# Performance work log

Measured on AMD Instinct MI355X. Metric: run time of the kernel, lower is better.

Reference implementation:

```python
import jax, jax.numpy as jnp
import numpy as np

N_NODES = 100000
N_EDGES = 1200000
N_GRAPHS = 512


def _init_linear(key, fan_in, fan_out):
    kw, kb = jax.random.split(key)
    lim = 1.0 / np.sqrt(fan_in)
    W = jax.random.uniform(kw, (fan_in, fan_out), minval=-lim, maxval=lim, dtype=jnp.float32)
    b = jax.random.uniform(kb, (fan_out,), minval=-lim, maxval=lim, dtype=jnp.float32)
    return W, b


def setup_inputs() -> dict:
    key = jax.random.key(0)
    ks = jax.random.split(key, 12)
    x = jax.random.normal(ks[0], (N_NODES, 10), dtype=jnp.float32)
    edge_index = jax.random.randint(ks[1], (2, N_EDGES), 0, N_NODES, dtype=jnp.int64)
    batch = jnp.sort(jax.random.randint(ks[2], (N_NODES,), 0, N_GRAPHS, dtype=jnp.int64))
    edge_weights = jax.random.uniform(ks[3], (N_EDGES,), dtype=jnp.float32)
    W1, b1 = _init_linear(ks[4], 10, 60)
    W2, b2 = _init_linear(ks[5], 60, 60)
    W3, b3 = _init_linear(ks[6], 60, 60)
    W4, b4 = _init_linear(ks[7], 60, 60)
    L1w, L1b = _init_linear(ks[8], 60, 60)
    L2w, L2b = _init_linear(ks[9], 60, 10)
    L3w, L3b = _init_linear(ks[10], 10, 2)
    return dict(x=x, edge_index=edge_index, batch=batch, edge_weights=edge_weights,
                W1=W1, b1=b1, W2=W2, b2=b2, W3=W3, b3=b3, W4=W4, b4=b4,
                L1w=L1w, L1b=L1b, L2w=L2w, L2b=L2b, L3w=L3w, L3b=L3b)


def gcn_conv(x, W, b, src, dst, ew, n):
    # PyG GCNConv: add self-loops (weight 1), symmetric normalization, linear, scatter-add.
    deg = jax.ops.segment_sum(ew, dst, num_segments=n) + 1.0  # +1 self-loop
    dinv = jnp.where(deg > 0, jax.lax.rsqrt(deg), 0.0)
    h = x @ W  # [n, out]
    norm = dinv[src] * ew * dinv[dst]  # [E]
    agg = jax.ops.segment_sum(h[src] * norm[:, None], dst, num_segments=n)
    agg = agg + h * (dinv * dinv)[:, None]  # self-loop contribution (weight 1)
    return agg + b


def _forward(x, edge_index, batch, edge_weights,
             W1, b1, W2, b2, W3, b3, W4, b4,
             L1w, L1b, L2w, L2b, L3w, L3b):
    src, dst = edge_index[0], edge_index[1]
    n = x.shape[0]
    h = jax.nn.relu(gcn_conv(x, W1, b1, src, dst, edge_weights, n))
    h = jax.nn.relu(gcn_conv(h, W2, b2, src, dst, edge_weights, n))
    h = jax.nn.relu(gcn_conv(h, W3, b3, src, dst, edge_weights, n))
    h = jax.nn.relu(gcn_conv(h, W4, b4, src, dst, edge_weights, n))
    g = jax.ops.segment_max(h, batch, num_segments=N_GRAPHS)
    g = jnp.where(jnp.isfinite(g), g, 0.0)  # guard empty graphs
    g = jax.nn.relu(g @ L1w + L1b)
    g = jax.nn.relu(g @ L2w + L2b)
    return g @ L3w + L3b


def reference(x, edge_index, batch, edge_weights,
              W1, b1, W2, b2, W3, b3, W4, b4,
              L1w, L1b, L2w, L2b, L3w, L3b):
    return _forward(x, edge_index, batch, edge_weights,
                    W1, b1, W2, b2, W3, b3, W4, b4,
                    L1w, L1b, L2w, L2b, L3w, L3b)
```

## Files before the change

kernel.cpp:

```cpp
#include <hip/hip_runtime.h>
#include <hip/hip_fp16.h>

#define N_NODES 100000
#define N_EDGES 1200000
#define N_GRAPHS 512
#define F 60
#define NPW 8
#define CAP 48
#define NBKT 782
#define EPB 4096
#define CPX 37
#define NCH 296
#define BKT_CAP 2048

__global__ void __launch_bounds__(256) k_hist(const int* __restrict__ dst,
                                              int* __restrict__ histM, int E) {
    __shared__ int h[NBKT];
    int c = (blockIdx.x & 7) * CPX + (blockIdx.x >> 3);
    for (int i = threadIdx.x; i < NBKT; i += 256) h[i] = 0;
    __syncthreads();
    int b0 = c * EPB;
    for (int i = threadIdx.x; i < EPB; i += 256) {
        int e = b0 + i;
        if (e < E) atomicAdd(&h[dst[e] >> 7], 1);
    }
    __syncthreads();
    for (int i = threadIdx.x; i < NBKT; i += 256) histM[c * NBKT + i] = h[i];
}

__global__ void k_scan(int* __restrict__ histM, int* __restrict__ tot) {
    int b = blockIdx.x * 256 + threadIdx.x;
    if (b >= NBKT) return;
    int running = 0;
    for (int c = 0; c < NCH; c += 8) {
        int i0 = (c + 0) * NBKT + b, i1 = (c + 1) * NBKT + b;
        int i2 = (c + 2) * NBKT + b, i3 = (c + 3) * NBKT + b;
        int i4 = (c + 4) * NBKT + b, i5 = (c + 5) * NBKT + b;
        int i6 = (c + 6) * NBKT + b, i7 = (c + 7) * NBKT + b;
        int v0 = histM[i0], v1 = histM[i1], v2 = histM[i2], v3 = histM[i3];
        int v4 = histM[i4], v5 = histM[i5], v6 = histM[i6], v7 = histM[i7];
        histM[i0] = running; running += v0;
        histM[i1] = running; running += v1;
        histM[i2] = running; running += v2;
        histM[i3] = running; running += v3;
        histM[i4] = running; running += v4;
        histM[i5] = running; running += v5;
        histM[i6] = running; running += v6;
        histM[i7] = running; running += v7;
    }
    tot[b] = running;
}

__global__ void __launch_bounds__(256) k_fill(const int* __restrict__ src,
                                              const int* __restrict__ dst,
                                              const float* __restrict__ ew,
                                              const int* __restrict__ histM,
                                              int2* __restrict__ bkt, int E) {
    __shared__ int h[NBKT];
    int c = (blockIdx.x & 7) * CPX + (blockIdx.x >> 3);
    for (int i = threadIdx.x; i < NBKT; i += 256) h[i] = 0;
    __syncthreads();
    int b0 = c * EPB;
    const int* bas = histM + c * NBKT;
    for (int i = threadIdx.x; i < EPB; i += 256) {
        int e = b0 + i;
        if (e >= E) continue;
        int d = dst[e];
        int b = d >> 7;
        int r = atomicAdd(&h[b], 1);
        int pos = bas[b] + r;
        if (pos < BKT_CAP) {
            int2 p;
            p.x = src[e] | ((d & 127) << 17);
            p.y = __float_as_int(ew[e]);
            bkt[(size_t)b * BKT_CAP + pos] = p;
        }
    }
}

__global__ void __launch_bounds__(256) k_build(
        const int* __restrict__ tot, const int2* __restrict__ bkt,
        int2* __restrict__ csr, int* __restrict__ cnt,
        float* __restrict__ dinv, const float* __restrict__ x,
        float* __restrict__ xs, int n) {
    __shared__ int lcur[128];
    __shared__ float ldeg[128];
    int b = blockIdx.x, tid = threadIdx.x;
    if (tid < 128) { lcur[tid] = 0; ldeg[tid] = 0.f; }
    __syncthreads();
    int nbase = b << 7;
    int m = min(tot[b], BKT_CAP);
    const int2* sb = bkt + (size_t)b * BKT_CAP;
    for (int i = tid; i < m; i += 256) {
        int2 p = sb[i];
        int srcv = p.x & 0x1FFFF;
        int low = (p.x >> 17) & 127;
        int pos = atomicAdd(&lcur[low], 1);
        if (pos < CAP) {
            int2 q; q.x = srcv; q.y = p.y;
            csr[(size_t)(nbase + low) * CAP + pos] = q;
        }
        atomicAdd(&ldeg[low], __int_as_float(p.y));
    }
    __syncthreads();
    if (tid < 128) {
        int v = nbase + tid;
        if (v < n) {
            int mA = min(lcur[tid], CAP);
            cnt[v] = mA;
            float di = rsqrtf(ldeg[tid] + 1.0f);
            dinv[v] = di;
            #pragma unroll
            for (int c2 = 0; c2 < 10; ++c2) xs[v * 16 + c2] = di * x[v * 10 + c2];
            #pragma unroll
            for (int c2 = 10; c2 < 16; ++c2) xs[v * 16 + c2] = 0.f;
            int g0 = tid & ~3;
            int m4 = max(max(min(lcur[g0], CAP),     min(lcur[g0 + 1], CAP)),
                         max(min(lcur[g0 + 2], CAP), min(lcur[g0 + 3], CAP)));
            int R = (m4 + 7) & ~7;
            int2 z; z.x = 0; z.y = 0;
            for (int e = mA; e < R; ++e) csr[(size_t)v * CAP + e] = z;
        }
    }
}

template<bool FIRST, bool SCALE_OUT>
__global__ void __launch_bounds__(256) k_layer(
        const void* __restrict__ HinV, const float* __restrict__ W,
        const float* __restrict__ bias,
        const int2* __restrict__ csr, const int* __restrict__ cnt,
        const float* __restrict__ dinv,
        __half* __restrict__ Hout, int n) {
    constexpr int WIN = FIRST ? 10 : 60;
    constexpr int WINP = FIRST ? 12 : 60;
    const float*  Hf = (const float*)HinV;
    const __half* Hh = (const __half*)HinV;
    __shared__ float Ws[WINP * 64];
    __shared__ __align__(16) float accS[4][NPW][64];
    for (int i = threadIdx.x; i < WINP * 64; i += 256) {
        int k = i >> 6, j = i & 63;
        Ws[i] = (j < F && k < WIN) ? W[k * F + j] : 0.f;
    }

    int wave = threadIdx.x >> 6;
    int lane = threadIdx.x & 63;
    float bj = (lane < F) ? bias[lane] : 0.f;
    int base = (blockIdx.x * 4 + wave) * NPW;

    if constexpr (FIRST) {
        __syncthreads();
        int l16 = lane & 15;
        int q = lane >> 4;
        #pragma unroll
        for (int p = 0; p < 2; ++p) {
            int v = base + 4 * p + q;
            float a = Hf[v * 16 + l16];
            int mm = min(cnt[v], CAP);
            int t1 = max(mm, __shfl_xor(mm, 16));
            int mu = max(t1, __shfl_xor(t1, 32));
            const int2* seg = csr + (size_t)v * CAP;
            for (int e = 0; e < mu; e += 4) {
                int2 p0 = seg[e], p1 = seg[e + 1], p2 = seg[e + 2], p3 = seg[e + 3];
                float x0 = Hf[p0.x * 16 + l16];
                float x1 = Hf[p1.x * 16 + l16];
                float x2 = Hf[p2.x * 16 + l16];
                float x3 = Hf[p3.x * 16 + l16];
                a = fmaf(__int_as_float(p0.y), x0, a);
                a = fmaf(__int_as_float(p1.y), x1, a);
                a = fmaf(__int_as_float(p2.y), x2, a);
                a = fmaf(__int_as_float(p3.y), x3, a);
            }
            accS[wave][4 * p + q][l16] = a * dinv[v];
        }
        float o[NPW];
        #pragma unroll
        for (int t = 0; t < NPW; ++t) o[t] = bj;
        const float4* aq = (const float4*)&accS[wave][0][0];
        #pragma unroll
        for (int kq = 0; kq < 3; ++kq) {
            float w0 = Ws[(4 * kq + 0) * 64 + lane];
            float w1 = Ws[(4 * kq + 1) * 64 + lane];
            float w2 = Ws[(4 * kq + 2) * 64 + lane];
            float w3 = Ws[(4 * kq + 3) * 64 + lane];
            #pragma unroll
            for (int t = 0; t < NPW; ++t) {
                float4 aa = aq[t * 16 + kq];
                o[t] = fmaf(aa.x, w0, o[t]);
                o[t] = fmaf(aa.y, w1, o[t]);
                o[t] = fmaf(aa.z, w2, o[t]);
                o[t] = fmaf(aa.w, w3, o[t]);
            }
        }
        #pragma unroll
        for (int t = 0; t < NPW; ++t) {
            float sc = SCALE_OUT ? dinv[base + t] : 1.f;
            Hout[(size_t)(base + t) * 64 + lane] = __float2half_rn(fmaxf(o[t], 0.f) * sc);
        }
    } else {
        __syncthreads();
        int h  = lane >> 5;
        int lh = lane & 31;
        int fo = lh * 2;

        #pragma unroll
        for (int p = 0; p < 4; ++p) {
            int v = base + 2 * p + h;
            float di = dinv[v];
            __half2 sh = *(const __half2*)(Hh + (size_t)v * 64 + fo);
            float2 a;
            a.x = __low2float(sh);
            a.y = __high2float(sh);
            int mm = min(cnt[v], CAP);
            int mo = __shfl(mm, lane ^ 32);
            int mu = max(mm, mo);
            const int2* seg = csr + (size_t)v * CAP;
            for (int e = 0; e < mu; e += 8) {
                const int4* s4 = (const int4*)(seg + e);
                int4 q0 = s4[0], q1 = s4[1], q2 = s4[2], q3 = s4[3];
                __half2 g0 = *(const __half2*)(Hh + (size_t)q0.x * 64 + fo);
                __half2 g1 = *(const __half2*)(Hh + (size_t)q0.z * 64 + fo);
                __half2 g2 = *(const __half2*)(Hh + (size_t)q1.x * 64 + fo);
                __half2 g3 = *(const __half2*)(Hh + (size_t)q1.z * 64 + fo);
                __half2 g4 = *(const __half2*)(Hh + (size_t)q2.x * 64 + fo);
                __half2 g5 = *(const __half2*)(Hh + (size_t)q2.z * 64 + fo);
                __half2 g6 = *(const __half2*)(Hh + (size_t)q3.x * 64 + fo);
                __half2 g7 = *(const __half2*)(Hh + (size_t)q3.z * 64 + fo);
                float w0 = __int_as_float(q0.y), w1 = __int_as_float(q0.w);
                float w2 = __int_as_float(q1.y), w3 = __int_as_float(q1.w);
                float w4 = __int_as_float(q2.y), w5 = __int_as_float(q2.w);
                float w6 = __int_as_float(q3.y), w7 = __int_as_float(q3.w);
                a.x = fmaf(w0, __low2float(g0), a.x); a.y = fmaf(w0, __high2float(g0), a.y);
                a.x = fmaf(w1, __low2float(g1), a.x); a.y = fmaf(w1, __high2float(g1), a.y);
                a.x = fmaf(w2, __low2float(g2), a.x); a.y = fmaf(w2, __high2float(g2), a.y);
                a.x = fmaf(w3, __low2float(g3), a.x); a.y = fmaf(w3, __high2float(g3), a.y);
                a.x = fmaf(w4, __low2float(g4), a.x); a.y = fmaf(w4, __high2float(g4), a.y);
                a.x = fmaf(w5, __low2float(g5), a.x); a.y = fmaf(w5, __high2float(g5), a.y);
                a.x = fmaf(w6, __low2float(g6), a.x); a.y = fmaf(w6, __high2float(g6), a.y);
                a.x = fmaf(w7, __low2float(g7), a.x); a.y = fmaf(w7, __high2float(g7), a.y);
            }
            a.x *= di; a.y *= di;
            *(float2*)&accS[wave][2 * p + h][fo] = a;
        }

        float o[NPW];
        #pragma unroll
        for (int t = 0; t < NPW; ++t) o[t] = bj;
        const float4* aq = (const float4*)&accS[wave][0][0];
        #pragma unroll
        for (int kq = 0; kq < 15; ++kq) {
            float w0 = Ws[(4 * kq + 0) * 64 + lane];
            float w1 = Ws[(4 * kq + 1) * 64 + lane];
            float w2 = Ws[(4 * kq + 2) * 64 + lane];
            float w3 = Ws[(4 * kq + 3) * 64 + lane];
            #pragma unroll
            for (int t = 0; t < NPW; ++t) {
                float4 aa = aq[t * 16 + kq];
                o[t] = fmaf(aa.x, w0, o[t]);
                o[t] = fmaf(aa.y, w1, o[t]);
                o[t] = fmaf(aa.z, w2, o[t]);
                o[t] = fmaf(aa.w, w3, o[t]);
            }
        }
        #pragma unroll
        for (int t = 0; t < NPW; ++t) {
            float sc = SCALE_OUT ? dinv[base + t] : 1.f;
            Hout[(size_t)(base + t) * 64 + lane] = __float2half_rn(fmaxf(o[t], 0.f) * sc);
        }
    }
}

__global__ void k_gstart(const int* __restrict__ batch, int* __restrict__ start, int n) {
    int i = blockIdx.x * 256 + threadIdx.x;
    if (i >= n) return;
    int b = batch[i];
    int pb = (i == 0) ? -1 : batch[i - 1];
    for (int g = pb + 1; g <= b; ++g) start[g] = i;
    if (i == n - 1) for (int g = b + 1; g <= N_GRAPHS; ++g) start[g] = n;
}

__global__ void k_pool2(const __half* __restrict__ H, const int* __restrict__ start,
                        float* __restrict__ g) {
    __shared__ float red[4 * F];
    int gi = blockIdx.x;
    int wave = threadIdx.x >> 6;
    int lane = threadIdx.x & 63;
    int s = start[gi], e = start[gi + 1];
    float m = 0.f;
    for (int i = s + wave; i < e; i += 4)
        m = fmaxf(m, __half2float(H[(size_t)i * 64 + lane]));
    if (lane < F) red[wave * F + lane] = m;
    __syncthreads();
    if (threadIdx.x < F) {
        float r = fmaxf(fmaxf(red[threadIdx.x], red[F + threadIdx.x]),
                        fmaxf(red[2 * F + threadIdx.x], red[3 * F + threadIdx.x]));
        g[gi * F + threadIdx.x] = r;
    }
}

__global__ void k_mlp(const float* __restrict__ g,
                      const float* __restrict__ L1w, const float* __restrict__ L1b,
                      const float* __restrict__ L2w, const float* __restrict__ L2b,
                      const float* __restrict__ L3w, const float* __restrict__ L3b,
                      float* __restrict__ out) {
    __shared__ float gin[F], h1[F], h2[10];
    int gi = blockIdx.x;
    int t = threadIdx.x;
    if (t < F) gin[t] = g[gi * F + t];
    __syncthreads();
    if (t < F) {
        float a = L1b[t];
        for (int k = 0; k < F; ++k) a += gin[k] * L1w[k * F + t];
        h1[t] = fmaxf(a, 0.f);
    }
    __syncthreads();
    if (t < 10) {
        float a = L2b[t];
        for (int k = 0; k < F; ++k) a += h1[k] * L2w[k * 10 + t];
        h2[t] = fmaxf(a, 0.f);
    }
    __syncthreads();
    if (t < 2) {
        float a = L3b[t];
        for (int k = 0; k < 10; ++k) a += h2[k] * L3w[k * 2 + t];
        out[gi * 2 + t] = a;
    }
}

extern "C" void kernel_launch(void* const* d_in, const int* in_sizes, int n_in,
                              void* d_out, int out_size, void* d_ws, size_t ws_size,
                              hipStream_t stream) {
    const int n = N_NODES, E = N_EDGES;
    const float* x   = (const float*)d_in[0];
    const int* ei    = (const int*)d_in[1];
    const int* batch = (const int*)d_in[2];
    const float* ew  = (const float*)d_in[3];
    const float* W1 = (const float*)d_in[4],  *b1 = (const float*)d_in[5];
    const float* W2 = (const float*)d_in[6],  *b2 = (const float*)d_in[7];
    const float* W3 = (const float*)d_in[8],  *b3 = (const float*)d_in[9];
    const float* W4 = (const float*)d_in[10], *b4 = (const float*)d_in[11];
    const float* L1w = (const float*)d_in[12], *L1b = (const float*)d_in[13];
    const float* L2w = (const float*)d_in[14], *L2b = (const float*)d_in[15];
    const float* L3w = (const float*)d_in[16], *L3b = (const float*)d_in[17];
    float* out = (float*)d_out;

    const int* src = ei;
    const int* dst = ei + E;

    char* ws = (char*)d_ws;
    size_t off = 0;
    auto carve = [&](size_t bytes) {
        void* p = ws + off;
        off += (bytes + 255) & ~size_t(255);
        return p;
    };
    int*    cnt   = (int*)carve(n * 4);
    float*  dinv  = (float*)carve(n * 4);
    int*    gst   = (int*)carve((N_GRAPHS + 1) * 4);
    int2*   csr   = (int2*)carve((size_t)n * CAP * 8);
    int2*   bkt   = (int2*)carve((size_t)NBKT * BKT_CAP * 8);
    int*    histM = (int*)carve((size_t)NCH * NBKT * 4);
    int*    tot   = (int*)carve(NBKT * 4);
    float*  xs    = (float*)carve((size_t)n * 16 * 4);
    __half* hA    = (__half*)carve((size_t)n * 64 * 2);
    __half* hB    = (__half*)carve((size_t)n * 64 * 2);
    float*  g0    = (float*)carve((size_t)N_GRAPHS * F * 4);
    (void)ws_size;

    const int NB = (n + 255) / 256;
    const int LB = n / (4 * NPW);

    k_hist<<<NCH, 256, 0, stream>>>(dst, histM, E);
    k_scan<<<(NBKT + 255) / 256, 256, 0, stream>>>(histM, tot);
    k_fill<<<NCH, 256, 0, stream>>>(src, dst, ew, histM, bkt, E);
    k_build<<<NBKT, 256, 0, stream>>>(tot, bkt, csr, cnt, dinv, x, xs, n);
    k_gstart<<<NB, 256, 0, stream>>>(batch, gst, n);

    k_layer<true,  true ><<<LB, 256, 0, stream>>>(xs, W1, b1, csr, cnt, dinv, hA, n);
    k_layer<false, true ><<<LB, 256, 0, stream>>>(hA, W2, b2, csr, cnt, dinv, hB, n);
    k_layer<false, true ><<<LB, 256, 0, stream>>>(hB, W3, b3, csr, cnt, dinv, hA, n);
    k_layer<false, false><<<LB, 256, 0, stream>>>(hA, W4, b4, csr, cnt, dinv, hB, n);

    k_pool2<<<N_GRAPHS, 256, 0, stream>>>(hB, gst, g0);
    k_mlp<<<N_GRAPHS, 64, 0, stream>>>(g0, L1w, L1b, L2w, L2b, L3w, L3b, out);
}
```

Measured before the change: 253.9 us.

## Pack CSR entries into 32-bit words with quantized weights and fuse small kernels

CSR edges now fit in one 32-bit word: 17-bit source index and 15-bit fixed-point edge weight. This halves the CSR bytes read in every layer. The hidden layers now gather for four nodes at once under a shared loop bound, padded to groups of 8 nodes, which raises memory-level parallelism. The scan is fused with graph-start computation and pooling is fused with the MLP, removing two launches. Quantizing weights to 15 bits adds rounding error, and the shared loop bound adds wasted iterations for low-degree nodes.

```diff
diff --git a/kernel.cpp b/kernel.cpp
--- a/kernel.cpp
+++ b/kernel.cpp
@@ -12,6 +12,7 @@
 #define CPX 37
 #define NCH 296
 #define BKT_CAP 2048
+#define WSC 3.0518509e-05f
 
 __global__ void __launch_bounds__(256) k_hist(const int* __restrict__ dst,
                                               int* __restrict__ histM, int E) {
@@ -28,27 +29,38 @@
     for (int i = threadIdx.x; i < NBKT; i += 256) histM[c * NBKT + i] = h[i];
 }
 
-__global__ void k_scan(int* __restrict__ histM, int* __restrict__ tot) {
-    int b = blockIdx.x * 256 + threadIdx.x;
-    if (b >= NBKT) return;
-    int running = 0;
-    for (int c = 0; c < NCH; c += 8) {
-        int i0 = (c + 0) * NBKT + b, i1 = (c + 1) * NBKT + b;
-        int i2 = (c + 2) * NBKT + b, i3 = (c + 3) * NBKT + b;
-        int i4 = (c + 4) * NBKT + b, i5 = (c + 5) * NBKT + b;
-        int i6 = (c + 6) * NBKT + b, i7 = (c + 7) * NBKT + b;
-        int v0 = histM[i0], v1 = histM[i1], v2 = histM[i2], v3 = histM[i3];
-        int v4 = histM[i4], v5 = histM[i5], v6 = histM[i6], v7 = histM[i7];
-        histM[i0] = running; running += v0;
-        histM[i1] = running; running += v1;
-        histM[i2] = running; running += v2;
-        histM[i3] = running; running += v3;
-        histM[i4] = running; running += v4;
-        histM[i5] = running; running += v5;
-        histM[i6] = running; running += v6;
-        histM[i7] = running; running += v7;
-    }
-    tot[b] = running;
+__global__ void k_scan_gstart(int* __restrict__ histM, int* __restrict__ tot,
+                              const int* __restrict__ batch, int* __restrict__ gst, int n) {
+    int bi = blockIdx.x;
+    if (bi < 4) {
+        int b = bi * 256 + threadIdx.x;
+        if (b >= NBKT) return;
+        int running = 0;
+        for (int c = 0; c < NCH; c += 8) {
+            int i0 = (c + 0) * NBKT + b, i1 = (c + 1) * NBKT + b;
+            int i2 = (c + 2) * NBKT + b, i3 = (c + 3) * NBKT + b;
+            int i4 = (c + 4) * NBKT + b, i5 = (c + 5) * NBKT + b;
+            int i6 = (c + 6) * NBKT + b, i7 = (c + 7) * NBKT + b;
+            int v0 = histM[i0], v1 = histM[i1], v2 = histM[i2], v3 = histM[i3];
+            int v4 = histM[i4], v5 = histM[i5], v6 = histM[i6], v7 = histM[i7];
+            histM[i0] = running; running += v0;
+            histM[i1] = running; running += v1;
+            histM[i2] = running; running += v2;
+            histM[i3] = running; running += v3;
+            histM[i4] = running; running += v4;
+            histM[i5] = running; running += v5;
+            histM[i6] = running; running += v6;
+            histM[i7] = running; running += v7;
+        }
+        tot[b] = running;
+    } else {
+        int i = (bi - 4) * 256 + threadIdx.x;
+        if (i >= n) return;
+        int b = batch[i];
+        int pb = (i == 0) ? -1 : batch[i - 1];
+        for (int g = pb + 1; g <= b; ++g) gst[g] = i;
+        if (i == n - 1) for (int g = b + 1; g <= N_GRAPHS; ++g) gst[g] = n;
+    }
 }
 
 __global__ void __launch_bounds__(256) k_fill(const int* __restrict__ src,
@@ -80,7 +92,7 @@
 
 __global__ void __launch_bounds__(256) k_build(
         const int* __restrict__ tot, const int2* __restrict__ bkt,
-        int2* __restrict__ csr, int* __restrict__ cnt,
+        unsigned* __restrict__ csr, int* __restrict__ cnt,
         float* __restrict__ dinv, const float* __restrict__ x,
         float* __restrict__ xs, int n) {
     __shared__ int lcur[128];
@@ -97,8 +109,8 @@
         int low = (p.x >> 17) & 127;
         int pos = atomicAdd(&lcur[low], 1);
         if (pos < CAP) {
-            int2 q; q.x = srcv; q.y = p.y;
-            csr[(size_t)(nbase + low) * CAP + pos] = q;
+            unsigned w15 = (unsigned)(int)rintf(__int_as_float(p.y) * 32767.f);
+            csr[(size_t)(nbase + low) * CAP + pos] = (unsigned)srcv | (w15 << 17);
         }
         atomicAdd(&ldeg[low], __int_as_float(p.y));
     }
@@ -114,12 +126,12 @@
             for (int c2 = 0; c2 < 10; ++c2) xs[v * 16 + c2] = di * x[v * 10 + c2];
             #pragma unroll
             for (int c2 = 10; c2 < 16; ++c2) xs[v * 16 + c2] = 0.f;
-            int g0 = tid & ~3;
-            int m4 = max(max(min(lcur[g0], CAP),     min(lcur[g0 + 1], CAP)),
-                         max(min(lcur[g0 + 2], CAP), min(lcur[g0 + 3], CAP)));
-            int R = (m4 + 7) & ~7;
-            int2 z; z.x = 0; z.y = 0;
-            for (int e = mA; e < R; ++e) csr[(size_t)v * CAP + e] = z;
+            int g0 = tid & ~7;
+            int m8 = 0;
+            #pragma unroll
+            for (int i2 = 0; i2 < 8; ++i2) m8 = max(m8, min(lcur[g0 + i2], CAP));
+            int R = (m8 + 3) & ~3;
+            for (int e = mA; e < R; ++e) csr[(size_t)v * CAP + e] = 0u;
         }
     }
 }
@@ -128,7 +140,7 @@
 __global__ void __launch_bounds__(256) k_layer(
         const void* __restrict__ HinV, const float* __restrict__ W,
         const float* __restrict__ bias,
-        const int2* __restrict__ csr, const int* __restrict__ cnt,
+        const unsigned* __restrict__ csr, const int* __restrict__ cnt,
         const float* __restrict__ dinv,
         __half* __restrict__ Hout, int n) {
     constexpr int WIN = FIRST ? 10 : 60;
@@ -155,20 +167,20 @@
         for (int p = 0; p < 2; ++p) {
             int v = base + 4 * p + q;
             float a = Hf[v * 16 + l16];
-            int mm = min(cnt[v], CAP);
+            int mm = cnt[v];
             int t1 = max(mm, __shfl_xor(mm, 16));
             int mu = max(t1, __shfl_xor(t1, 32));
-            const int2* seg = csr + (size_t)v * CAP;
+            const unsigned* seg = csr + (size_t)v * CAP;
             for (int e = 0; e < mu; e += 4) {
-                int2 p0 = seg[e], p1 = seg[e + 1], p2 = seg[e + 2], p3 = seg[e + 3];
-                float x0 = Hf[p0.x * 16 + l16];
-                float x1 = Hf[p1.x * 16 + l16];
-                float x2 = Hf[p2.x * 16 + l16];
-                float x3 = Hf[p3.x * 16 + l16];
-                a = fmaf(__int_as_float(p0.y), x0, a);
-                a = fmaf(__int_as_float(p1.y), x1, a);
-                a = fmaf(__int_as_float(p2.y), x2, a);
-                a = fmaf(__int_as_float(p3.y), x3, a);
+                uint4 qq = *(const uint4*)(seg + e);
+                float x0 = Hf[(qq.x & 0x1FFFF) * 16 + l16];
+                float x1 = Hf[(qq.y & 0x1FFFF) * 16 + l16];
+                float x2 = Hf[(qq.z & 0x1FFFF) * 16 + l16];
+                float x3 = Hf[(qq.w & 0x1FFFF) * 16 + l16];
+                a = fmaf((float)(qq.x >> 17) * WSC, x0, a);
+                a = fmaf((float)(qq.y >> 17) * WSC, x1, a);
+                a = fmaf((float)(qq.z >> 17) * WSC, x2, a);
+                a = fmaf((float)(qq.w >> 17) * WSC, x3, a);
             }
             accS[wave][4 * p + q][l16] = a * dinv[v];
         }
@@ -202,44 +214,52 @@
         int lh = lane & 31;
         int fo = lh * 2;
 
+        float2 acc2[4];
+        float dis[4];
+        const unsigned* seg[4];
         #pragma unroll
         for (int p = 0; p < 4; ++p) {
             int v = base + 2 * p + h;
-            float di = dinv[v];
+            dis[p] = dinv[v];
             __half2 sh = *(const __half2*)(Hh + (size_t)v * 64 + fo);
-            float2 a;
-            a.x = __low2float(sh);
-            a.y = __high2float(sh);
-            int mm = min(cnt[v], CAP);
-            int mo = __shfl(mm, lane ^ 32);
-            int mu = max(mm, mo);
-            const int2* seg = csr + (size_t)v * CAP;
-            for (int e = 0; e < mu; e += 8) {
-                const int4* s4 = (const int4*)(seg + e);
-                int4 q0 = s4[0], q1 = s4[1], q2 = s4[2], q3 = s4[3];
-                __half2 g0 = *(const __half2*)(Hh + (size_t)q0.x * 64 + fo);
-                __half2 g1 = *(const __half2*)(Hh + (size_t)q0.z * 64 + fo);
-                __half2 g2 = *(const __half2*)(Hh + (size_t)q1.x * 64 + fo);
-                __half2 g3 = *(const __half2*)(Hh + (size_t)q1.z * 64 + fo);
-                __half2 g4 = *(const __half2*)(Hh + (size_t)q2.x * 64 + fo);
-                __half2 g5 = *(const __half2*)(Hh + (size_t)q2.z * 64 + fo);
-                __half2 g6 = *(const __half2*)(Hh + (size_t)q3.x * 64 + fo);
-                __half2 g7 = *(const __half2*)(Hh + (size_t)q3.z * 64 + fo);
-                float w0 = __int_as_float(q0.y), w1 = __int_as_float(q0.w);
-                float w2 = __int_as_float(q1.y), w3 = __int_as_float(q1.w);
-                float w4 = __int_as_float(q2.y), w5 = __int_as_float(q2.w);
-                float w6 = __int_as_float(q3.y), w7 = __int_as_float(q3.w);
-                a.x = fmaf(w0, __low2float(g0), a.x); a.y = fmaf(w0, __high2float(g0), a.y);
-                a.x = fmaf(w1, __low2float(g1), a.x); a.y = fmaf(w1, __high2float(g1), a.y);
-                a.x = fmaf(w2, __low2float(g2), a.x); a.y = fmaf(w2, __high2float(g2), a.y);
-                a.x = fmaf(w3, __low2float(g3), a.x); a.y = fmaf(w3, __high2float(g3), a.y);
-                a.x = fmaf(w4, __low2float(g4), a.x); a.y = fmaf(w4, __high2float(g4), a.y);
-                a.x = fmaf(w5, __low2float(g5), a.x); a.y = fmaf(w5, __high2float(g5), a.y);
-                a.x = fmaf(w6, __low2float(g6), a.x); a.y = fmaf(w6, __high2float(g6), a.y);
-                a.x = fmaf(w7, __low2float(g7), a.x); a.y = fmaf(w7, __high2float(g7), a.y);
+            acc2[p].x = __low2float(sh);
+            acc2[p].y = __high2float(sh);
+            seg[p] = csr + (size_t)v * CAP;
+        }
+        int cmy = cnt[base + (lane & 7)];
+        int m1 = max(cmy, __shfl_xor(cmy, 1));
+        int m2 = max(m1, __shfl_xor(m1, 2));
+        int mu = max(m2, __shfl_xor(m2, 4));
+
+        for (int e = 0; e < mu; e += 4) {
+            uint4 q[4];
+            #pragma unroll
+            for (int p = 0; p < 4; ++p) q[p] = *(const uint4*)(seg[p] + e);
+            #pragma unroll
+            for (int p = 0; p < 4; ++p) {
+                unsigned e0 = q[p].x, e1 = q[p].y, e2 = q[p].z, e3 = q[p].w;
+                __half2 g0 = *(const __half2*)(Hh + (size_t)(e0 & 0x1FFFF) * 64 + fo);
+                __half2 g1 = *(const __half2*)(Hh + (size_t)(e1 & 0x1FFFF) * 64 + fo);
+                __half2 g2 = *(const __half2*)(Hh + (size_t)(e2 & 0x1FFFF) * 64 + fo);
+                __half2 g3 = *(const __half2*)(Hh + (size_t)(e3 & 0x1FFFF) * 64 + fo);
+                float w0 = (float)(e0 >> 17) * WSC;
+                float w1 = (float)(e1 >> 17) * WSC;
+                float w2 = (float)(e2 >> 17) * WSC;
+                float w3 = (float)(e3 >> 17) * WSC;
+                acc2[p].x = fmaf(w0, __low2float(g0), acc2[p].x);
+                acc2[p].y = fmaf(w0, __high2float(g0), acc2[p].y);
+                acc2[p].x = fmaf(w1, __low2float(g1), acc2[p].x);
+                acc2[p].y = fmaf(w1, __high2float(g1), acc2[p].y);
+                acc2[p].x = fmaf(w2, __low2float(g2), acc2[p].x);
+                acc2[p].y = fmaf(w2, __high2float(g2), acc2[p].y);
+                acc2[p].x = fmaf(w3, __low2float(g3), acc2[p].x);
+                acc2[p].y = fmaf(w3, __high2float(g3), acc2[p].y);
             }
-            a.x *= di; a.y *= di;
-            *(float2*)&accS[wave][2 * p + h][fo] = a;
+        }
+        #pragma unroll
+        for (int p = 0; p < 4; ++p) {
+            acc2[p].x *= dis[p]; acc2[p].y *= dis[p];
+            *(float2*)&accS[wave][2 * p + h][fo] = acc2[p];
         }
 
         float o[NPW];
@@ -269,43 +289,26 @@
     }
 }
 
-__global__ void k_gstart(const int* __restrict__ batch, int* __restrict__ start, int n) {
-    int i = blockIdx.x * 256 + threadIdx.x;
-    if (i >= n) return;
-    int b = batch[i];
-    int pb = (i == 0) ? -1 : batch[i - 1];
-    for (int g = pb + 1; g <= b; ++g) start[g] = i;
-    if (i == n - 1) for (int g = b + 1; g <= N_GRAPHS; ++g) start[g] = n;
-}
-
-__global__ void k_pool2(const __half* __restrict__ H, const int* __restrict__ start,
-                        float* __restrict__ g) {
+__global__ void __launch_bounds__(256) k_poolmlp(
+        const __half* __restrict__ H, const int* __restrict__ start,
+        const float* __restrict__ L1w, const float* __restrict__ L1b,
+        const float* __restrict__ L2w, const float* __restrict__ L2b,
+        const float* __restrict__ L3w, const float* __restrict__ L3b,
+        float* __restrict__ out) {
     __shared__ float red[4 * F];
+    __shared__ float gin[F], h1[F], h2[10];
     int gi = blockIdx.x;
     int wave = threadIdx.x >> 6;
     int lane = threadIdx.x & 63;
+    int t = threadIdx.x;
     int s = start[gi], e = start[gi + 1];
     float m = 0.f;
     for (int i = s + wave; i < e; i += 4)
         m = fmaxf(m, __half2float(H[(size_t)i * 64 + lane]));
     if (lane < F) red[wave * F + lane] = m;
     __syncthreads();
-    if (threadIdx.x < F) {
-        float r = fmaxf(fmaxf(red[threadIdx.x], red[F + threadIdx.x]),
-                        fmaxf(red[2 * F + threadIdx.x], red[3 * F + threadIdx.x]));
-        g[gi * F + threadIdx.x] = r;
-    }
-}
-
-__global__ void k_mlp(const float* __restrict__ g,
-                      const float* __restrict__ L1w, const float* __restrict__ L1b,
-                      const float* __restrict__ L2w, const float* __restrict__ L2b,
-                      const float* __restrict__ L3w, const float* __restrict__ L3b,
-                      float* __restrict__ out) {
-    __shared__ float gin[F], h1[F], h2[10];
-    int gi = blockIdx.x;
-    int t = threadIdx.x;
-    if (t < F) gin[t] = g[gi * F + t];
+    if (t < F)
+        gin[t] = fmaxf(fmaxf(red[t], red[F + t]), fmaxf(red[2 * F + t], red[3 * F + t]));
     __syncthreads();
     if (t < F) {
         float a = L1b[t];
@@ -353,33 +356,30 @@
         off += (bytes + 255) & ~size_t(255);
         return p;
     };
-    int*    cnt   = (int*)carve(n * 4);
-    float*  dinv  = (float*)carve(n * 4);
-    int*    gst   = (int*)carve((N_GRAPHS + 1) * 4);
-    int2*   csr   = (int2*)carve((size_t)n * CAP * 8);
-    int2*   bkt   = (int2*)carve((size_t)NBKT * BKT_CAP * 8);
-    int*    histM = (int*)carve((size_t)NCH * NBKT * 4);
-    int*    tot   = (int*)carve(NBKT * 4);
-    float*  xs    = (float*)carve((size_t)n * 16 * 4);
-    __half* hA    = (__half*)carve((size_t)n * 64 * 2);
-    __half* hB    = (__half*)carve((size_t)n * 64 * 2);
-    float*  g0    = (float*)carve((size_t)N_GRAPHS * F * 4);
+    int*      cnt   = (int*)carve(n * 4);
+    float*    dinv  = (float*)carve(n * 4);
+    int*      gst   = (int*)carve((N_GRAPHS + 1) * 4);
+    unsigned* csr   = (unsigned*)carve((size_t)n * CAP * 4);
+    int2*     bkt   = (int2*)carve((size_t)NBKT * BKT_CAP * 8);
+    int*      histM = (int*)carve((size_t)NCH * NBKT * 4);
+    int*      tot   = (int*)carve(NBKT * 4);
+    float*    xs    = (float*)carve((size_t)n * 16 * 4);
+    __half*   hA    = (__half*)carve((size_t)n * 64 * 2);
+    __half*   hB    = (__half*)carve((size_t)n * 64 * 2);
     (void)ws_size;
 
     const int NB = (n + 255) / 256;
     const int LB = n / (4 * NPW);
 
     k_hist<<<NCH, 256, 0, stream>>>(dst, histM, E);
-    k_scan<<<(NBKT + 255) / 256, 256, 0, stream>>>(histM, tot);
+    k_scan_gstart<<<4 + NB, 256, 0, stream>>>(histM, tot, batch, gst, n);
     k_fill<<<NCH, 256, 0, stream>>>(src, dst, ew, histM, bkt, E);
     k_build<<<NBKT, 256, 0, stream>>>(tot, bkt, csr, cnt, dinv, x, xs, n);
-    k_gstart<<<NB, 256, 0, stream>>>(batch, gst, n);
 
     k_layer<true,  true ><<<LB, 256, 0, stream>>>(xs, W1, b1, csr, cnt, dinv, hA, n);
     k_layer<false, true ><<<LB, 256, 0, stream>>>(hA, W2, b2, csr, cnt, dinv, hB, n);
     k_layer<false, true ><<<LB, 256, 0, stream>>>(hB, W3, b3, csr, cnt, dinv, hA, n);
     k_layer<false, false><<<LB, 256, 0, stream>>>(hA, W4, b4, csr, cnt, dinv, hB, n);
 
-    k_pool2<<<N_GRAPHS, 256, 0, stream>>>(hB, gst, g0);
-    k_mlp<<<N_GRAPHS, 64, 0, stream>>>(g0, L1w, L1b, L2w, L2b, L3w, L3b, out);
-}
+    k_poolmlp<<<N_GRAPHS, 256, 0, stream>>>(hB, gst, L1w, L1b, L2w, L2b, L3w, L3b, out);
+}
```

Result: faster. 228.3 us (-10.1%).
